# Optimization experiments

Hardware: AMD Instinct MI355X
Metric: run time of the kernel (lower is better)

Reference implementation:

```python
import jax, jax.numpy as jnp
import numpy as np

D_MODEL = 2048
N_HEADS = 16
D_HEAD = 128
ROPE_BASE = 10000.0


def _rope(q, k, start_pos):
    # q, k: [B, H, S, Dh]; standard rotate-half RoPE
    S, Dh = q.shape[-2], q.shape[-1]
    inv_freq = 1.0 / (ROPE_BASE ** (jnp.arange(0, Dh, 2, dtype=jnp.float32) / Dh))  # [Dh/2]
    pos = jnp.arange(S, dtype=jnp.float32) + start_pos                              # [S]
    ang = pos[:, None] * inv_freq[None, :]                                          # [S, Dh/2]
    cos = jnp.concatenate([jnp.cos(ang), jnp.cos(ang)], axis=-1)[None, None]        # [1,1,S,Dh]
    sin = jnp.concatenate([jnp.sin(ang), jnp.sin(ang)], axis=-1)[None, None]

    def rot_half(t):
        t1, t2 = jnp.split(t, 2, axis=-1)
        return jnp.concatenate([-t2, t1], axis=-1)

    return q * cos + rot_half(q) * sin, k * cos + rot_half(k) * sin


def setup_inputs() -> dict:
    key = jax.random.key(0)
    k1, k2, k3 = jax.random.split(key, 3)
    B, S = 2, 2048
    scale_in = 1.0 / np.sqrt(D_MODEL)
    x = jax.random.normal(k1, (B, S, D_MODEL), dtype=jnp.float32)
    w_qkv = jax.random.normal(k2, (3 * D_MODEL, D_MODEL), dtype=jnp.float32) * scale_in
    w_out = jax.random.normal(k3, (D_MODEL, D_MODEL), dtype=jnp.float32) * scale_in
    return {"x": x, "w_qkv": w_qkv, "w_out": w_out, "start_pos": 0}


def reference(x, w_qkv, w_out, start_pos):
    B, S, _ = x.shape
    scale = 1.0 / np.sqrt(D_HEAD)
    qkv = jnp.einsum('bsd,ed->bse', x, w_qkv)                 # [B,S,3D]
    q, k, v = jnp.split(qkv, 3, axis=-1)
    # [B,S,D] -> [B,H,S,Dh]
    reshape = lambda t: t.reshape(B, S, N_HEADS, D_HEAD).transpose(0, 2, 1, 3)
    q, k, v = reshape(q), reshape(k), reshape(v)
    q, k = _rope(q, k, start_pos)
    scores = jnp.einsum('bhqd,bhkd->bhqk', q, k) * scale      # [B,H,S,S]
    if S > 1:
        causal = jnp.tril(jnp.ones((S, S), dtype=bool))
        scores = jnp.where(causal[None, None], scores, -jnp.inf)
    attn = jax.nn.softmax(scores, axis=-1)
    out = jnp.einsum('bhqk,bhkd->bhqd', attn, v)              # [B,H,S,Dh]
    out = out.transpose(0, 2, 1, 3).reshape(B, S, D_MODEL)
    return jnp.einsum('bsd,ed->bse', out, w_out)
```

## Files before the change

kernel.cpp:

```cpp
#include <hip/hip_runtime.h>

typedef unsigned short ushort;
typedef __attribute__((ext_vector_type(8))) short short8;
typedef __attribute__((ext_vector_type(4))) float f32x4;

#define NH 16
#define DH 128
#define SEQ 2048
#define DMODEL 2048
#define GK 2048

__device__ __forceinline__ ushort f2bf(float f) {
  union { float f; unsigned u; } v; v.f = f;
  unsigned u = v.u;
  unsigned r = (u + 0x7fffu + ((u >> 16) & 1u)) >> 16;
  return (ushort)r;
}
__device__ __forceinline__ float bf2f(ushort h) {
  union { unsigned u; float f; } v; v.u = ((unsigned)h) << 16; return v.f;
}

__device__ __forceinline__ void async16(const ushort* g, ushort* l) {
  __builtin_amdgcn_global_load_lds(
      (const __attribute__((address_space(1))) unsigned*)g,
      (__attribute__((address_space(3))) unsigned*)l, 16, 0, 0);
}

#define NX  2097152
#define NWQ 3145728
#define NWO 1048576
__global__ void cast3_kernel(const float* __restrict__ x, const float* __restrict__ wq,
                             const float* __restrict__ wo, ushort* __restrict__ xb,
                             ushort* __restrict__ wqb, ushort* __restrict__ wob) {
  int i = blockIdx.x * blockDim.x + threadIdx.x;
  int stride = gridDim.x * blockDim.x;
  for (; i < NX + NWQ + NWO; i += stride) {
    const float* s; ushort* d; int j;
    if (i < NX)            { s = x;  d = xb;  j = i; }
    else if (i < NX + NWQ) { s = wq; d = wqb; j = i - NX; }
    else                   { s = wo; d = wob; j = i - NX - NWQ; }
    float4 v = ((const float4*)s)[j];
    unsigned long long p = (unsigned long long)f2bf(v.x)
                         | ((unsigned long long)f2bf(v.y) << 16)
                         | ((unsigned long long)f2bf(v.z) << 32)
                         | ((unsigned long long)f2bf(v.w) << 48);
    ((unsigned long long*)d)[j] = p;
  }
}

template<int MODE, int NTK, int BN>
__global__ __launch_bounds__(512, 1)
void gemmk(const ushort* __restrict__ A, const ushort* __restrict__ B, int N,
           ushort* __restrict__ oq, ushort* __restrict__ ok, ushort* __restrict__ ov,
           float* __restrict__ of, float* __restrict__ of2) {
  constexpr int NF = BN / 64;
  constexpr int WN = BN / 4;
  __shared__ ushort As[2][256 * 64];
  __shared__ ushort Bs[2][BN * 64];
  const int tid = threadIdx.x;
  const int lane = tid & 63;
  const int w = tid >> 6;
  const int wm = w >> 2, wn = w & 3;
  const int g = lane >> 4, l16 = lane & 15;
  const int m0 = blockIdx.y * 256;
  const int n0 = blockIdx.x * BN;
  const int kb = (int)blockIdx.z * (NTK * 64);
  const ushort* Ablk = A + (size_t)m0 * GK;
  const ushort* Bblk = B + (size_t)n0 * GK;

  const int r0 = tid >> 3, sl = tid & 7;
  const int gcol = ((sl * 16) ^ ((r0 & 7) << 4)) >> 1;
  const int ldsb = r0 * 64 + sl * 8;

  f32x4 acc[8][NF];
#pragma unroll
  for (int mf = 0; mf < 8; ++mf)
#pragma unroll
    for (int nf = 0; nf < NF; ++nf) acc[mf][nf] = (f32x4)0.f;

  short8 ra[4], rb[NF];
#pragma unroll
  for (int j = 0; j < 4; ++j)
    ra[j] = *(const short8*)(Ablk + (size_t)(j * 64 + r0) * GK + kb + gcol);
#pragma unroll
  for (int j = 0; j < NF; ++j)
    rb[j] = *(const short8*)(Bblk + (size_t)(j * 64 + r0) * GK + kb + gcol);
#pragma unroll
  for (int j = 0; j < 4; ++j) *(short8*)&As[0][j * 4096 + ldsb] = ra[j];
#pragma unroll
  for (int j = 0; j < NF; ++j) *(short8*)&Bs[0][j * 4096 + ldsb] = rb[j];
#pragma unroll
  for (int j = 0; j < 4; ++j)
    ra[j] = *(const short8*)(Ablk + (size_t)(j * 64 + r0) * GK + kb + 64 + gcol);
#pragma unroll
  for (int j = 0; j < NF; ++j)
    rb[j] = *(const short8*)(Bblk + (size_t)(j * 64 + r0) * GK + kb + 64 + gcol);
#pragma unroll
  for (int j = 0; j < 4; ++j) *(short8*)&As[1][j * 4096 + ldsb] = ra[j];
#pragma unroll
  for (int j = 0; j < NF; ++j) *(short8*)&Bs[1][j * 4096 + ldsb] = rb[j];
  __syncthreads();

  for (int t = 0; t < NTK; ++t) {
    const bool pre = (t + 2 < NTK);
    if (pre) {
      const int kt = kb + (t + 2) * 64;
#pragma unroll
      for (int j = 0; j < 4; ++j)
        ra[j] = *(const short8*)(Ablk + (size_t)(j * 64 + r0) * GK + kt + gcol);
#pragma unroll
      for (int j = 0; j < NF; ++j)
        rb[j] = *(const short8*)(Bblk + (size_t)(j * 64 + r0) * GK + kt + gcol);
    }
    __builtin_amdgcn_sched_barrier(0);

    const ushort* cA = As[t & 1];
    const ushort* cB = Bs[t & 1];
    short8 bfr[NF][2];
#pragma unroll
    for (int nf = 0; nf < NF; ++nf) {
      int row = wn * WN + nf * 16 + l16;
#pragma unroll
      for (int ks = 0; ks < 2; ++ks)
        bfr[nf][ks] = *(const short8*)&cB[row * 64 + (((ks * 64 + g * 16) ^ ((l16 & 7) << 4)) >> 1)];
    }
#pragma unroll
    for (int p = 0; p < 4; ++p) {
      short8 af[2][2];
#pragma unroll
      for (int mi = 0; mi < 2; ++mi) {
        int row = wm * 128 + (2 * p + mi) * 16 + l16;
#pragma unroll
        for (int ks = 0; ks < 2; ++ks)
          af[mi][ks] = *(const short8*)&cA[row * 64 + (((ks * 64 + g * 16) ^ ((l16 & 7) << 4)) >> 1)];
      }
      __builtin_amdgcn_s_setprio(1);
#pragma unroll
      for (int mi = 0; mi < 2; ++mi)
#pragma unroll
        for (int nf = 0; nf < NF; ++nf)
#pragma unroll
          for (int ks = 0; ks < 2; ++ks)
            acc[2 * p + mi][nf] = __builtin_amdgcn_mfma_f32_16x16x32_bf16(
                af[mi][ks], bfr[nf][ks], acc[2 * p + mi][nf], 0, 0, 0);
      __builtin_amdgcn_s_setprio(0);
    }

    __syncthreads();
    if (pre) {
      ushort* nA = (ushort*)As[t & 1];
      ushort* nB = (ushort*)Bs[t & 1];
#pragma unroll
      for (int j = 0; j < 4; ++j) *(short8*)&nA[j * 4096 + ldsb] = ra[j];
#pragma unroll
      for (int j = 0; j < NF; ++j) *(short8*)&nB[j * 4096 + ldsb] = rb[j];
    }
  }

#pragma unroll
  for (int mf = 0; mf < 8; ++mf)
#pragma unroll
    for (int nf = 0; nf < NF; ++nf)
#pragma unroll
      for (int i = 0; i < 4; ++i) {
        int row = m0 + wm * 128 + mf * 16 + g * 4 + i;
        int col = n0 + wn * WN + nf * 16 + l16;
        float val = acc[mf][nf][i];
        if (MODE == 0) {
          int which = col >> 11;
          int r = col & 2047;
          int h = r >> 7, dh = r & 127;
          int b = row >> 11, s = row & 2047;
          size_t dst = ((size_t)(b * NH + h) * SEQ + s) * DH + dh;
          ushort* o = (which == 0) ? oq : (which == 1 ? ok : ov);
          o[dst] = f2bf(val);
        } else {
          float* d = blockIdx.z ? of2 : of;
          d[(size_t)row * N + col] = val;
        }
      }
}

__global__ void addf4_kernel(float* __restrict__ out, const float* __restrict__ part, int n4) {
  int i = blockIdx.x * blockDim.x + threadIdx.x;
  int stride = gridDim.x * blockDim.x;
  for (; i < n4; i += stride) {
    float4 a = ((const float4*)out)[i];
    float4 b = ((const float4*)part)[i];
    a.x += b.x; a.y += b.y; a.z += b.z; a.w += b.w;
    ((float4*)out)[i] = a;
  }
}

__global__ void rope_kernel(ushort* __restrict__ q, ushort* __restrict__ k,
                            const int* __restrict__ spp) {
  int id = blockIdx.x * blockDim.x + threadIdx.x;
  int j = id & 63;
  int s = (id >> 6) & (SEQ - 1);
  int bh = id >> 17;
  size_t base = ((size_t)bh * SEQ + s) * DH;
  float pos = (float)(s + spp[0]);
  float ang = pos * __expf(-(float)j * (9.210340371976184f / 64.f));
  float c = cosf(ang), sn = sinf(ang);
  float q1 = bf2f(q[base + j]), q2 = bf2f(q[base + 64 + j]);
  q[base + j]      = f2bf(q1 * c - q2 * sn);
  q[base + 64 + j] = f2bf(q2 * c + q1 * sn);
  float k1 = bf2f(k[base + j]), k2 = bf2f(k[base + 64 + j]);
  k[base + j]      = f2bf(k1 * c - k2 * sn);
  k[base + 64 + j] = f2bf(k2 * c + k1 * sn);
}

__global__ __launch_bounds__(256, 2)
void attn_kernel(const ushort* __restrict__ Q, const ushort* __restrict__ K,
                 const ushort* __restrict__ V, ushort* __restrict__ O) {
  __shared__ ushort Ks[2][64 * 128];
  __shared__ ushort Vt[2][128 * 72];
  __shared__ ushort Ps[4][16 * 72];
  const int tid = threadIdx.x;
  const int lane = tid & 63;
  const int w = tid >> 6;
  const int g = lane >> 4, l16 = lane & 15;
  const int h = blockIdx.y, b = blockIdx.z;
  const int bh = b * NH + h;
  const ushort* Qb = Q + (size_t)bh * SEQ * DH;
  const ushort* Kb = K + (size_t)bh * SEQ * DH;
  const ushort* Vb = V + (size_t)bh * SEQ * DH;
  const float scale = 0.08838834764831845f;

  const int vkv = (tid >> 3) * 2;
  const int vd0 = (tid & 7) * 16;
  const int vmask = (tid & 7) << 3;

  for (int pass = 0; pass < 2; ++pass) {
    const int qt = pass == 0 ? (31 - (int)blockIdx.x) : (int)blockIdx.x;
    const int q0 = qt * 64;
    const int nkt = qt + 1;

    short8 qf[4];
    {
      const ushort* qrow = Qb + (size_t)(q0 + w * 16 + l16) * DH;
#pragma unroll
      for (int ks = 0; ks < 4; ++ks) qf[ks] = *(const short8*)(qrow + ks * 32 + g * 8);
    }
    f32x4 oacc[8];
#pragma unroll
    for (int i = 0; i < 8; ++i) oacc[i] = (f32x4)0.f;
    float m_i[4], l_i[4];
#pragma unroll
    for (int i = 0; i < 4; ++i) { m_i[i] = -INFINITY; l_i[i] = 0.f; }

#pragma unroll
    for (int it = 0; it < 4; ++it) {
      int ci = it * 256 + tid;
      int row = ci >> 4;
      int cb = ((ci & 15) * 16) ^ ((row & 7) << 4);
      async16(Kb + (size_t)row * DH + (cb >> 1), &Ks[0][ci * 8]);
    }
    {
      short8 vr[4];
      vr[0] = *(const short8*)(Vb + (size_t)vkv * DH + vd0);
      vr[1] = *(const short8*)(Vb + (size_t)vkv * DH + vd0 + 8);
      vr[2] = *(const short8*)(Vb + (size_t)(vkv + 1) * DH + vd0);
      vr[3] = *(const short8*)(Vb + (size_t)(vkv + 1) * DH + vd0 + 8);
#pragma unroll
      for (int j = 0; j < 16; ++j) {
        int d = vd0 + j;
        const ushort* a = (const ushort*)&vr[j >> 3];
        const ushort* c = (const ushort*)&vr[2 + (j >> 3)];
        unsigned val = (unsigned)a[j & 7] | ((unsigned)c[j & 7] << 16);
        *(unsigned*)&Vt[0][d * 72 + (vkv ^ vmask)] = val;
      }
    }
    __syncthreads();

    int cur = 0;
    for (int t = 0; t < nkt; ++t) {
      const int k0 = t * 64;
      const int nxt = cur ^ 1;
      const bool pre = (t + 1 < nkt);
      short8 vr[4];
      if (pre) {
        const int kn = (t + 1) * 64;
#pragma unroll
        for (int it = 0; it < 4; ++it) {
          int ci = it * 256 + tid;
          int row = ci >> 4;
          int cb = ((ci & 15) * 16) ^ ((row & 7) << 4);
          async16(Kb + (size_t)(kn + row) * DH + (cb >> 1), &Ks[nxt][ci * 8]);
        }
        vr[0] = *(const short8*)(Vb + (size_t)(kn + vkv) * DH + vd0);
        vr[1] = *(const short8*)(Vb + (size_t)(kn + vkv) * DH + vd0 + 8);
        vr[2] = *(const short8*)(Vb + (size_t)(kn + vkv + 1) * DH + vd0);
        vr[3] = *(const short8*)(Vb + (size_t)(kn + vkv + 1) * DH + vd0 + 8);
      }

      f32x4 sacc[4];
#pragma unroll
      for (int nf = 0; nf < 4; ++nf) sacc[nf] = (f32x4)0.f;
      __builtin_amdgcn_s_setprio(1);
#pragma unroll
      for (int nf = 0; nf < 4; ++nf) {
        int row = nf * 16 + l16;
#pragma unroll
        for (int ks = 0; ks < 4; ++ks) {
          int cb = (ks * 64 + g * 16) ^ ((l16 & 7) << 4);
          short8 kf = *(const short8*)&Ks[cur][row * 128 + (cb >> 1)];
          sacc[nf] = __builtin_amdgcn_mfma_f32_16x16x32_bf16(qf[ks], kf, sacc[nf], 0, 0, 0);
        }
      }
      __builtin_amdgcn_s_setprio(0);

      float pv[4][4], mxr[4];
#pragma unroll
      for (int i = 0; i < 4; ++i)
#pragma unroll
        for (int nf = 0; nf < 4; ++nf) pv[i][nf] = sacc[nf][i] * scale;
      if (t == nkt - 1) {
#pragma unroll
        for (int i = 0; i < 4; ++i) {
          int qrow = q0 + w * 16 + g * 4 + i;
#pragma unroll
          for (int nf = 0; nf < 4; ++nf)
            if (k0 + nf * 16 + l16 > qrow) pv[i][nf] = -INFINITY;
        }
      }
#pragma unroll
      for (int i = 0; i < 4; ++i) {
        float mx = fmaxf(fmaxf(pv[i][0], pv[i][1]), fmaxf(pv[i][2], pv[i][3]));
#pragma unroll
        for (int d = 1; d < 16; d <<= 1) mx = fmaxf(mx, __shfl_xor(mx, d, 64));
        mxr[i] = mx;
      }
      int need = 0;
#pragma unroll
      for (int i = 0; i < 4; ++i) need |= (mxr[i] > m_i[i] + 8.f) ? 1 : 0;
      if (__any(need)) {
#pragma unroll
        for (int i = 0; i < 4; ++i) {
          float mnew = fmaxf(m_i[i], mxr[i]);
          float alpha = __expf(m_i[i] - mnew);
          l_i[i] *= alpha;
          m_i[i] = mnew;
#pragma unroll
          for (int nf2 = 0; nf2 < 8; ++nf2) oacc[nf2][i] *= alpha;
        }
      }
#pragma unroll
      for (int i = 0; i < 4; ++i) {
        float p[4], sum = 0.f;
#pragma unroll
        for (int nf = 0; nf < 4; ++nf) { p[nf] = __expf(pv[i][nf] - m_i[i]); sum += p[nf]; }
#pragma unroll
        for (int d = 1; d < 16; d <<= 1) sum += __shfl_xor(sum, d, 64);
        l_i[i] += sum;
#pragma unroll
        for (int nf = 0; nf < 4; ++nf)
          Ps[w][(g * 4 + i) * 72 + nf * 16 + l16] = f2bf(p[nf]);
      }
      __asm__ volatile("s_waitcnt lgkmcnt(0)" ::: "memory");
      __builtin_amdgcn_sched_barrier(0);

      __builtin_amdgcn_s_setprio(1);
#pragma unroll
      for (int kvh = 0; kvh < 2; ++kvh) {
        short8 pa = *(const short8*)&Ps[w][l16 * 72 + kvh * 32 + g * 8];
#pragma unroll
        for (int nf2 = 0; nf2 < 8; ++nf2) {
          int cb = (kvh * 32 + g * 8) ^ (nf2 * 8);
          short8 vf = *(const short8*)&Vt[cur][(nf2 * 16 + l16) * 72 + cb];
          oacc[nf2] = __builtin_amdgcn_mfma_f32_16x16x32_bf16(pa, vf, oacc[nf2], 0, 0, 0);
        }
      }
      __builtin_amdgcn_s_setprio(0);

      if (pre) {
#pragma unroll
        for (int j = 0; j < 16; ++j) {
          int d = vd0 + j;
          const ushort* a = (const ushort*)&vr[j >> 3];
          const ushort* c = (const ushort*)&vr[2 + (j >> 3)];
          unsigned val = (unsigned)a[j & 7] | ((unsigned)c[j & 7] << 16);
          *(unsigned*)&Vt[nxt][d * 72 + (vkv ^ vmask)] = val;
        }
      }
      __syncthreads();
      cur = nxt;
    }

#pragma unroll
    for (int i = 0; i < 4; ++i) {
      float inv = 1.f / l_i[i];
      int row = q0 + w * 16 + g * 4 + i;
      size_t obase = ((size_t)b * SEQ + row) * DMODEL + h * DH;
#pragma unroll
      for (int nf2 = 0; nf2 < 8; ++nf2)
        O[obase + nf2 * 16 + l16] = f2bf(oacc[nf2][i] * inv);
    }
  }
}

extern "C" void kernel_launch(void* const* d_in, const int* in_sizes, int n_in,
                              void* d_out, int out_size, void* d_ws, size_t ws_size,
                              hipStream_t stream) {
  const float* x    = (const float*)d_in[0];
  const float* wqkv = (const float*)d_in[1];
  const float* wout = (const float*)d_in[2];
  const int*   spp  = (const int*)d_in[3];
  float* out = (float*)d_out;

  ushort* ws = (ushort*)d_ws;
  ushort* xb  = ws;
  ushort* wqb = xb + 8388608;
  ushort* wob = wqb + 12582912;
  ushort* q   = wob + 4194304;
  ushort* k   = q + 8388608;
  ushort* v   = k + 8388608;
  ushort* ao  = v + 8388608;

  cast3_kernel<<<2048, 256, 0, stream>>>(x, wqkv, wout, xb, wqb, wob);

  gemmk<0, 32, 192><<<dim3(6144 / 192, 4096 / 256, 1), 512, 0, stream>>>(
      xb, wqb, 6144, q, k, v, nullptr, nullptr);

  rope_kernel<<<4194304 / 256, 256, 0, stream>>>(q, k, spp);

  attn_kernel<<<dim3(16, NH, 2), 256, 0, stream>>>(q, k, v, ao);

  float* part = (float*)q;
  gemmk<1, 16, 256><<<dim3(2048 / 256, 4096 / 256, 2), 512, 0, stream>>>(
      ao, wob, 2048, nullptr, nullptr, nullptr, out, part);
  addf4_kernel<<<2048, 256, 0, stream>>>(out, part, 2097152);
}
```

Baseline: 281.9 us.

## Double attention query tile to 128 rows with 8 waves per block

Attention blocks now process 128 query rows with 512 threads (8 waves), each K/V tile loaded to LDS being shared by twice as many rows. Waves whose rows lie entirely before a K tile skip compute for that tile, and causal masking is applied per wave. This aims to halve K/V global loads and V transpose work per query, at the cost of fewer blocks and idle waves on diagonal tiles.

```diff
diff --git a/kernel.cpp b/kernel.cpp
--- a/kernel.cpp
+++ b/kernel.cpp
@@ -210,12 +210,12 @@
   k[base + 64 + j] = f2bf(k2 * c + k1 * sn);
 }
 
-__global__ __launch_bounds__(256, 2)
+__global__ __launch_bounds__(512, 1)
 void attn_kernel(const ushort* __restrict__ Q, const ushort* __restrict__ K,
                  const ushort* __restrict__ V, ushort* __restrict__ O) {
   __shared__ ushort Ks[2][64 * 128];
   __shared__ ushort Vt[2][128 * 72];
-  __shared__ ushort Ps[4][16 * 72];
+  __shared__ ushort Ps[8][16 * 72];
   const int tid = threadIdx.x;
   const int lane = tid & 63;
   const int w = tid >> 6;
@@ -227,18 +227,19 @@
   const ushort* Vb = V + (size_t)bh * SEQ * DH;
   const float scale = 0.08838834764831845f;
 
-  const int vkv = (tid >> 3) * 2;
-  const int vd0 = (tid & 7) * 16;
-  const int vmask = (tid & 7) << 3;
+  const int vkv = (tid >> 4) * 2;
+  const int vd0 = (tid & 15) * 8;
+  const int vmask = ((vd0 >> 4) & 7) << 3;
 
   for (int pass = 0; pass < 2; ++pass) {
-    const int qt = pass == 0 ? (31 - (int)blockIdx.x) : (int)blockIdx.x;
-    const int q0 = qt * 64;
-    const int nkt = qt + 1;
+    const int qt = pass == 0 ? (15 - (int)blockIdx.x) : (int)blockIdx.x;
+    const int q0 = qt * 128;
+    const int nkt = 2 * qt + 2;
+    const int rbase = q0 + w * 16;
 
     short8 qf[4];
     {
-      const ushort* qrow = Qb + (size_t)(q0 + w * 16 + l16) * DH;
+      const ushort* qrow = Qb + (size_t)(rbase + l16) * DH;
 #pragma unroll
       for (int ks = 0; ks < 4; ++ks) qf[ks] = *(const short8*)(qrow + ks * 32 + g * 8);
     }
@@ -250,25 +251,21 @@
     for (int i = 0; i < 4; ++i) { m_i[i] = -INFINITY; l_i[i] = 0.f; }
 
 #pragma unroll
-    for (int it = 0; it < 4; ++it) {
-      int ci = it * 256 + tid;
+    for (int it = 0; it < 2; ++it) {
+      int ci = it * 512 + tid;
       int row = ci >> 4;
       int cb = ((ci & 15) * 16) ^ ((row & 7) << 4);
       async16(Kb + (size_t)row * DH + (cb >> 1), &Ks[0][ci * 8]);
     }
     {
-      short8 vr[4];
-      vr[0] = *(const short8*)(Vb + (size_t)vkv * DH + vd0);
-      vr[1] = *(const short8*)(Vb + (size_t)vkv * DH + vd0 + 8);
-      vr[2] = *(const short8*)(Vb + (size_t)(vkv + 1) * DH + vd0);
-      vr[3] = *(const short8*)(Vb + (size_t)(vkv + 1) * DH + vd0 + 8);
-#pragma unroll
-      for (int j = 0; j < 16; ++j) {
-        int d = vd0 + j;
-        const ushort* a = (const ushort*)&vr[j >> 3];
-        const ushort* c = (const ushort*)&vr[2 + (j >> 3)];
-        unsigned val = (unsigned)a[j & 7] | ((unsigned)c[j & 7] << 16);
-        *(unsigned*)&Vt[0][d * 72 + (vkv ^ vmask)] = val;
+      short8 va = *(const short8*)(Vb + (size_t)vkv * DH + vd0);
+      short8 vc = *(const short8*)(Vb + (size_t)(vkv + 1) * DH + vd0);
+      const ushort* a = (const ushort*)&va;
+      const ushort* c = (const ushort*)&vc;
+#pragma unroll
+      for (int j = 0; j < 8; ++j) {
+        unsigned val = (unsigned)a[j] | ((unsigned)c[j] << 16);
+        *(unsigned*)&Vt[0][(vd0 + j) * 72 + (vkv ^ vmask)] = val;
       }
     }
     __syncthreads();
@@ -278,109 +275,108 @@
       const int k0 = t * 64;
       const int nxt = cur ^ 1;
       const bool pre = (t + 1 < nkt);
-      short8 vr[4];
+      short8 va, vc;
       if (pre) {
         const int kn = (t + 1) * 64;
 #pragma unroll
-        for (int it = 0; it < 4; ++it) {
-          int ci = it * 256 + tid;
+        for (int it = 0; it < 2; ++it) {
+          int ci = it * 512 + tid;
           int row = ci >> 4;
           int cb = ((ci & 15) * 16) ^ ((row & 7) << 4);
           async16(Kb + (size_t)(kn + row) * DH + (cb >> 1), &Ks[nxt][ci * 8]);
         }
-        vr[0] = *(const short8*)(Vb + (size_t)(kn + vkv) * DH + vd0);
-        vr[1] = *(const short8*)(Vb + (size_t)(kn + vkv) * DH + vd0 + 8);
-        vr[2] = *(const short8*)(Vb + (size_t)(kn + vkv + 1) * DH + vd0);
-        vr[3] = *(const short8*)(Vb + (size_t)(kn + vkv + 1) * DH + vd0 + 8);
-      }
-
-      f32x4 sacc[4];
-#pragma unroll
-      for (int nf = 0; nf < 4; ++nf) sacc[nf] = (f32x4)0.f;
-      __builtin_amdgcn_s_setprio(1);
-#pragma unroll
-      for (int nf = 0; nf < 4; ++nf) {
-        int row = nf * 16 + l16;
-#pragma unroll
-        for (int ks = 0; ks < 4; ++ks) {
-          int cb = (ks * 64 + g * 16) ^ ((l16 & 7) << 4);
-          short8 kf = *(const short8*)&Ks[cur][row * 128 + (cb >> 1)];
-          sacc[nf] = __builtin_amdgcn_mfma_f32_16x16x32_bf16(qf[ks], kf, sacc[nf], 0, 0, 0);
-        }
-      }
-      __builtin_amdgcn_s_setprio(0);
-
-      float pv[4][4], mxr[4];
-#pragma unroll
-      for (int i = 0; i < 4; ++i)
-#pragma unroll
-        for (int nf = 0; nf < 4; ++nf) pv[i][nf] = sacc[nf][i] * scale;
-      if (t == nkt - 1) {
+        va = *(const short8*)(Vb + (size_t)(kn + vkv) * DH + vd0);
+        vc = *(const short8*)(Vb + (size_t)(kn + vkv + 1) * DH + vd0);
+      }
+
+      if (k0 <= rbase + 15) {
+        f32x4 sacc[4];
+#pragma unroll
+        for (int nf = 0; nf < 4; ++nf) sacc[nf] = (f32x4)0.f;
+        __builtin_amdgcn_s_setprio(1);
+#pragma unroll
+        for (int nf = 0; nf < 4; ++nf) {
+          int row = nf * 16 + l16;
+#pragma unroll
+          for (int ks = 0; ks < 4; ++ks) {
+            int cb = (ks * 64 + g * 16) ^ ((l16 & 7) << 4);
+            short8 kf = *(const short8*)&Ks[cur][row * 128 + (cb >> 1)];
+            sacc[nf] = __builtin_amdgcn_mfma_f32_16x16x32_bf16(qf[ks], kf, sacc[nf], 0, 0, 0);
+          }
+        }
+        __builtin_amdgcn_s_setprio(0);
+
+        float pv[4][4], mxr[4];
+#pragma unroll
+        for (int i = 0; i < 4; ++i)
+#pragma unroll
+          for (int nf = 0; nf < 4; ++nf) pv[i][nf] = sacc[nf][i] * scale;
+        if (k0 + 63 > rbase) {
+#pragma unroll
+          for (int i = 0; i < 4; ++i) {
+            int qrow = rbase + g * 4 + i;
+#pragma unroll
+            for (int nf = 0; nf < 4; ++nf)
+              if (k0 + nf * 16 + l16 > qrow) pv[i][nf] = -INFINITY;
+          }
+        }
 #pragma unroll
         for (int i = 0; i < 4; ++i) {
-          int qrow = q0 + w * 16 + g * 4 + i;
+          float mx = fmaxf(fmaxf(pv[i][0], pv[i][1]), fmaxf(pv[i][2], pv[i][3]));
+#pragma unroll
+          for (int d = 1; d < 16; d <<= 1) mx = fmaxf(mx, __shfl_xor(mx, d, 64));
+          mxr[i] = mx;
+        }
+        int need = 0;
+#pragma unroll
+        for (int i = 0; i < 4; ++i) need |= (mxr[i] > m_i[i] + 8.f) ? 1 : 0;
+        if (__any(need)) {
+#pragma unroll
+          for (int i = 0; i < 4; ++i) {
+            float mnew = fmaxf(m_i[i], mxr[i]);
+            float alpha = __expf(m_i[i] - mnew);
+            l_i[i] *= alpha;
+            m_i[i] = mnew;
+#pragma unroll
+            for (int nf2 = 0; nf2 < 8; ++nf2) oacc[nf2][i] *= alpha;
+          }
+        }
+#pragma unroll
+        for (int i = 0; i < 4; ++i) {
+          float p[4], sum = 0.f;
+#pragma unroll
+          for (int nf = 0; nf < 4; ++nf) { p[nf] = __expf(pv[i][nf] - m_i[i]); sum += p[nf]; }
+#pragma unroll
+          for (int d = 1; d < 16; d <<= 1) sum += __shfl_xor(sum, d, 64);
+          l_i[i] += sum;
 #pragma unroll
           for (int nf = 0; nf < 4; ++nf)
-            if (k0 + nf * 16 + l16 > qrow) pv[i][nf] = -INFINITY;
-        }
-      }
-#pragma unroll
-      for (int i = 0; i < 4; ++i) {
-        float mx = fmaxf(fmaxf(pv[i][0], pv[i][1]), fmaxf(pv[i][2], pv[i][3]));
-#pragma unroll
-        for (int d = 1; d < 16; d <<= 1) mx = fmaxf(mx, __shfl_xor(mx, d, 64));
-        mxr[i] = mx;
-      }
-      int need = 0;
-#pragma unroll
-      for (int i = 0; i < 4; ++i) need |= (mxr[i] > m_i[i] + 8.f) ? 1 : 0;
-      if (__any(need)) {
-#pragma unroll
-        for (int i = 0; i < 4; ++i) {
-          float mnew = fmaxf(m_i[i], mxr[i]);
-          float alpha = __expf(m_i[i] - mnew);
-          l_i[i] *= alpha;
-          m_i[i] = mnew;
-#pragma unroll
-          for (int nf2 = 0; nf2 < 8; ++nf2) oacc[nf2][i] *= alpha;
-        }
-      }
-#pragma unroll
-      for (int i = 0; i < 4; ++i) {
-        float p[4], sum = 0.f;
-#pragma unroll
-        for (int nf = 0; nf < 4; ++nf) { p[nf] = __expf(pv[i][nf] - m_i[i]); sum += p[nf]; }
-#pragma unroll
-        for (int d = 1; d < 16; d <<= 1) sum += __shfl_xor(sum, d, 64);
-        l_i[i] += sum;
-#pragma unroll
-        for (int nf = 0; nf < 4; ++nf)
-          Ps[w][(g * 4 + i) * 72 + nf * 16 + l16] = f2bf(p[nf]);
-      }
-      __asm__ volatile("s_waitcnt lgkmcnt(0)" ::: "memory");
-      __builtin_amdgcn_sched_barrier(0);
-
-      __builtin_amdgcn_s_setprio(1);
-#pragma unroll
-      for (int kvh = 0; kvh < 2; ++kvh) {
-        short8 pa = *(const short8*)&Ps[w][l16 * 72 + kvh * 32 + g * 8];
-#pragma unroll
-        for (int nf2 = 0; nf2 < 8; ++nf2) {
-          int cb = (kvh * 32 + g * 8) ^ (nf2 * 8);
-          short8 vf = *(const short8*)&Vt[cur][(nf2 * 16 + l16) * 72 + cb];
-          oacc[nf2] = __builtin_amdgcn_mfma_f32_16x16x32_bf16(pa, vf, oacc[nf2], 0, 0, 0);
-        }
-      }
-      __builtin_amdgcn_s_setprio(0);
+            Ps[w][(g * 4 + i) * 72 + nf * 16 + l16] = f2bf(p[nf]);
+        }
+        __asm__ volatile("s_waitcnt lgkmcnt(0)" ::: "memory");
+        __builtin_amdgcn_sched_barrier(0);
+
+        __builtin_amdgcn_s_setprio(1);
+#pragma unroll
+        for (int kvh = 0; kvh < 2; ++kvh) {
+          short8 pa = *(const short8*)&Ps[w][l16 * 72 + kvh * 32 + g * 8];
+#pragma unroll
+          for (int nf2 = 0; nf2 < 8; ++nf2) {
+            int cb = (kvh * 32 + g * 8) ^ (nf2 * 8);
+            short8 vf = *(const short8*)&Vt[cur][(nf2 * 16 + l16) * 72 + cb];
+            oacc[nf2] = __builtin_amdgcn_mfma_f32_16x16x32_bf16(pa, vf, oacc[nf2], 0, 0, 0);
+          }
+        }
+        __builtin_amdgcn_s_setprio(0);
+      }
 
       if (pre) {
-#pragma unroll
-        for (int j = 0; j < 16; ++j) {
-          int d = vd0 + j;
-          const ushort* a = (const ushort*)&vr[j >> 3];
-          const ushort* c = (const ushort*)&vr[2 + (j >> 3)];
-          unsigned val = (unsigned)a[j & 7] | ((unsigned)c[j & 7] << 16);
-          *(unsigned*)&Vt[nxt][d * 72 + (vkv ^ vmask)] = val;
+        const ushort* a = (const ushort*)&va;
+        const ushort* c = (const ushort*)&vc;
+#pragma unroll
+        for (int j = 0; j < 8; ++j) {
+          unsigned val = (unsigned)a[j] | ((unsigned)c[j] << 16);
+          *(unsigned*)&Vt[nxt][(vd0 + j) * 72 + (vkv ^ vmask)] = val;
         }
       }
       __syncthreads();
@@ -390,7 +386,7 @@
 #pragma unroll
     for (int i = 0; i < 4; ++i) {
       float inv = 1.f / l_i[i];
-      int row = q0 + w * 16 + g * 4 + i;
+      int row = rbase + g * 4 + i;
       size_t obase = ((size_t)b * SEQ + row) * DMODEL + h * DH;
 #pragma unroll
       for (int nf2 = 0; nf2 < 8; ++nf2)
@@ -424,7 +420,7 @@
 
   rope_kernel<<<4194304 / 256, 256, 0, stream>>>(q, k, spp);
 
-  attn_kernel<<<dim3(16, NH, 2), 256, 0, stream>>>(q, k, v, ao);
+  attn_kernel<<<dim3(8, NH, 2), 512, 0, stream>>>(q, k, v, ao);
 
   float* part = (float*)q;
   gemmk<1, 16, 256><<<dim3(2048 / 256, 4096 / 256, 2), 512, 0, stream>>>(
```

New measurement: 287.2 us. No clear change (+1.9%).
